# Kernel optimization log

Measured on AMD Instinct MI355X. Metric: run time of the kernel, lower is better.

The kernel has to match this reference:

```python
import jax, jax.numpy as jnp
import numpy as np

N_NODES = 50000
N_EDGES = 800000
IN_CH = 64
HID_CH = 64
OUT_CH = 64
NUM_GRAPHS = 256


def setup_inputs() -> dict:
    key = jax.random.key(0)
    ks = jax.random.split(key, 9)
    x = jax.random.normal(ks[0], (N_NODES, IN_CH), dtype=jnp.float32)
    edge_index = jax.random.randint(ks[1], (2, N_EDGES), 0, N_NODES, dtype=jnp.int64)
    batch = jnp.sort(jax.random.randint(ks[2], (N_NODES,), 0, NUM_GRAPHS, dtype=jnp.int64))
    def glorot(k, fan_in, fan_out):
        s = jnp.sqrt(6.0 / (fan_in + fan_out))
        return jax.random.uniform(k, (fan_in, fan_out), jnp.float32, -s, s)
    W1 = glorot(ks[3], IN_CH, HID_CH)
    b1 = jnp.zeros((HID_CH,), jnp.float32)
    W2 = glorot(ks[4], HID_CH, HID_CH)
    b2 = jnp.zeros((HID_CH,), jnp.float32)
    W3 = glorot(ks[5], HID_CH, OUT_CH)
    b3 = jnp.zeros((OUT_CH,), jnp.float32)
    return {"x": x, "edge_index": edge_index, "batch": batch,
            "W1": W1, "b1": b1, "W2": W2, "b2": b2, "W3": W3, "b3": b3}


def gcn_conv(x, src, dst, W, b):
    # PyG GCNConv: linear, add self-loops, symmetric deg normalization, scatter-add, bias
    n = x.shape[0]
    xw = x @ W                                   # [N, F_out]
    loops = jnp.arange(n, dtype=src.dtype)
    s = jnp.concatenate([src, loops])            # sources (with self loops)
    d = jnp.concatenate([dst, loops])            # targets (with self loops)
    ones = jnp.ones(d.shape, dtype=x.dtype)
    deg = jax.ops.segment_sum(ones, d, num_segments=n)
    dinv = jnp.where(deg > 0, jax.lax.rsqrt(deg), 0.0)
    norm = dinv[s] * dinv[d]                     # [E + N]
    msgs = norm[:, None] * xw[s]                 # gather + scale
    out = jax.ops.segment_sum(msgs, d, num_segments=n)
    return out + b


def reference(x, edge_index, batch, W1, b1, W2, b2, W3, b3):
    src, dst = edge_index[0], edge_index[1]
    h = jax.nn.relu(gcn_conv(x, src, dst, W1, b1))
    h = jax.nn.relu(gcn_conv(h, src, dst, W2, b2))
    h = gcn_conv(h, src, dst, W3, b3)
    # global_add_pool over graph ids
    pooled = jax.ops.segment_sum(h, batch, num_segments=NUM_GRAPHS)  # [G, OUT_CH]
    return pooled  # out_channels != 1, so no flatten
```

## Files before the change

### kernel.cpp

```cpp
#include <hip/hip_runtime.h>
#include <hip/hip_bf16.h>

#define N_NODES 50000
#define N_EDGES 800000
#define CH 64
#define N_GRAPHS 256
#define NBUCK 196
#define CHUNK 4096
#define NHIST 98

__device__ __forceinline__ unsigned bf16_rne(float f) {
    unsigned u = __float_as_uint(f);
    return (u + 0x7fffu + ((u >> 16) & 1u)) >> 16;
}
__device__ __forceinline__ float4 ldtab(const unsigned short* __restrict__ tab, int s, int c4) {
    uint2 u = *(const uint2*)(tab + ((size_t)s << 6) + c4);
    float4 r;
    r.x = __uint_as_float(u.x << 16);
    r.y = __uint_as_float(u.x & 0xffff0000u);
    r.z = __uint_as_float(u.y << 16);
    r.w = __uint_as_float(u.y & 0xffff0000u);
    return r;
}

__global__ void edge_hist(const int* __restrict__ ei, int* __restrict__ hpart) {
    __shared__ int h[NBUCK];
    for (int i = threadIdx.x; i < NBUCK; i += 256) h[i] = 0;
    __syncthreads();
    int t = blockIdx.x * 256 + threadIdx.x;
    int stride = NHIST * 256 * 4;
    for (int e = t * 4; e < N_EDGES; e += stride) {
        int4 d = *(const int4*)&ei[N_EDGES + e];
        atomicAdd(&h[d.x >> 8], 1);
        atomicAdd(&h[d.y >> 8], 1);
        atomicAdd(&h[d.z >> 8], 1);
        atomicAdd(&h[d.w >> 8], 1);
    }
    __syncthreads();
    for (int i = threadIdx.x; i < NBUCK; i += 256)
        hpart[blockIdx.x * NBUCK + i] = h[i];
}

__global__ void bucket_scan(const int* __restrict__ hpart, int* __restrict__ bstart,
                            int* __restrict__ gcur, float* __restrict__ poolz) {
    int i = blockIdx.x * 256 + threadIdx.x;
    if (i < N_GRAPHS * CH + N_GRAPHS) poolz[i] = 0.0f;
    if (blockIdx.x != 0) return;
    __shared__ int sc[256];
    int tid = threadIdx.x;
    int v = 0;
    if (tid < NBUCK)
        for (int r = 0; r < NHIST; ++r) v += hpart[r * NBUCK + tid];
    sc[tid] = v;
    __syncthreads();
    for (int off = 1; off < 256; off <<= 1) {
        int t = (tid >= off) ? sc[tid - off] : 0;
        __syncthreads();
        sc[tid] += t;
        __syncthreads();
    }
    if (tid < NBUCK) {
        int ex = sc[tid] - v;
        bstart[tid] = ex;
        gcur[tid] = ex;
    }
    if (tid == 255) bstart[NBUCK] = sc[255];
}

__global__ __launch_bounds__(512) void bin_scatter(const int* __restrict__ ei,
                                                   int* __restrict__ gcur,
                                                   int2* __restrict__ ebuf) {
    __shared__ int hist[NBUCK];
    __shared__ int lofs[NBUCK];
    __shared__ int gbase[NBUCK];
    __shared__ int cur[NBUCK];
    __shared__ int sc[512];
    __shared__ int2 stage[CHUNK];
    int tid = threadIdx.x;
    for (int i = tid; i < NBUCK; i += 512) hist[i] = 0;
    __syncthreads();
    int e0 = blockIdx.x * CHUNK;
    int n = min(CHUNK, N_EDGES - e0);
    int src[8], dst[8];
#pragma unroll
    for (int k = 0; k < 8; ++k) {
        int idx = k * 512 + tid;
        if (idx < n) {
            int e = e0 + idx;
            src[k] = ei[e];
            dst[k] = ei[N_EDGES + e];
            atomicAdd(&hist[dst[k] >> 8], 1);
        } else dst[k] = -1;
    }
    __syncthreads();
    int v = (tid < NBUCK) ? hist[tid] : 0;
    sc[tid] = v;
    __syncthreads();
    for (int off = 1; off < 512; off <<= 1) {
        int t = (tid >= off) ? sc[tid - off] : 0;
        __syncthreads();
        sc[tid] += t;
        __syncthreads();
    }
    if (tid < NBUCK) {
        int ex = sc[tid] - v;
        lofs[tid] = ex;
        cur[tid] = ex;
        gbase[tid] = v ? atomicAdd(&gcur[tid], v) : 0;
    }
    __syncthreads();
#pragma unroll
    for (int k = 0; k < 8; ++k) {
        if (dst[k] >= 0) {
            int p = atomicAdd(&cur[dst[k] >> 8], 1);
            stage[p] = make_int2(src[k], dst[k]);
        }
    }
    __syncthreads();
    for (int i = tid; i < n; i += 512) {
        int2 p = stage[i];
        int b = p.y >> 8;
        ebuf[gbase[b] + (i - lofs[b])] = p;
    }
}

__global__ void csr_bucket(const int2* __restrict__ ebuf, const int* __restrict__ bstart,
                           int* __restrict__ deg, int* __restrict__ rowp,
                           float* __restrict__ dinv, int* __restrict__ col) {
    __shared__ int nd[256];
    __shared__ int cur[256];
    __shared__ int sc[256];
    int b = blockIdx.x;
    int tid = threadIdx.x;
    nd[tid] = 0;
    __syncthreads();
    int es = bstart[b], ee = bstart[b + 1];
    for (int e = es + tid; e < ee; e += 256)
        atomicAdd(&nd[ebuf[e].y & 255], 1);
    __syncthreads();
    int v = nd[tid];
    sc[tid] = v;
    __syncthreads();
    for (int off = 1; off < 256; off <<= 1) {
        int t = (tid >= off) ? sc[tid - off] : 0;
        __syncthreads();
        sc[tid] += t;
        __syncthreads();
    }
    int node = b * 256 + tid;
    int lstart = es + sc[tid] - v;
    if (node < N_NODES) {
        deg[node] = v;
        rowp[node] = lstart;
        dinv[node] = rsqrtf((float)v + 1.0f);
    }
    cur[tid] = lstart;
    __syncthreads();
    for (int e = es + tid; e < ee; e += 256) {
        int2 p = ebuf[e];
        int pos = atomicAdd(&cur[p.y & 255], 1);
        col[pos] = p.x;
    }
}

__global__ void gemm_reg(const float* __restrict__ in, const float* __restrict__ W,
                         unsigned short* __restrict__ out, int n) {
    __shared__ float WT[64 * 68];
    int tid = threadIdx.x;
    for (int i = tid; i < 64 * 64; i += 256) {
        int k = i >> 6, c = i & 63;
        WT[c * 68 + k] = W[i];
    }
    __syncthreads();
    int lane = tid & 63;
    int wv = __builtin_amdgcn_readfirstlane(tid >> 6);
    int row0 = blockIdx.x * 32 + wv * 8;
    if (row0 >= n) return;
    float acc[8] = {0.f, 0.f, 0.f, 0.f, 0.f, 0.f, 0.f, 0.f};
#pragma unroll 2
    for (int k = 0; k < 64; k += 4) {
        float4 w = *(const float4*)&WT[lane * 68 + k];
#pragma unroll
        for (int r = 0; r < 8; ++r) {
            float4 xv = *(const float4*)&in[(size_t)(row0 + r) * 64 + k];
            acc[r] = fmaf(xv.x, w.x, acc[r]);
            acc[r] = fmaf(xv.y, w.y, acc[r]);
            acc[r] = fmaf(xv.z, w.z, acc[r]);
            acc[r] = fmaf(xv.w, w.w, acc[r]);
        }
    }
#pragma unroll
    for (int r = 0; r < 8; ++r)
        out[(size_t)(row0 + r) * 64 + lane] = (unsigned short)bf16_rne(acc[r]);
}

template <int OUT_BF16, int USE_NRM, int WRITE_NRM>
__global__ void agg_v4(const int* __restrict__ rowp, const int* __restrict__ deg,
                       const int* __restrict__ col, const float* __restrict__ dinv,
                       float* nrm,
                       const unsigned short* __restrict__ tab, const float* __restrict__ bias,
                       void* __restrict__ outv, int do_relu) {
    int wv = __builtin_amdgcn_readfirstlane(threadIdx.x >> 6);
    int node = blockIdx.x * 4 + wv;
    int lane = threadIdx.x & 63;
    int q = lane >> 4;
    int c4 = (lane & 15) << 2;
    float dd = dinv[node];
    int cnt = deg[node];
    int start = rowp[node];
    float4 acc = make_float4(0.f, 0.f, 0.f, 0.f);
    if (q == 0) {
        float4 xs = ldtab(tab, node, c4);
        float dd2 = dd * dd;
        acc.x = xs.x * dd2; acc.y = xs.y * dd2; acc.z = xs.z * dd2; acc.w = xs.w * dd2;
    }
    int j = 0;
    for (; j + 8 <= cnt; j += 8) {
        int sA = col[start + j + q];
        int sB = col[start + j + 4 + q];
        float nA, nB;
        if (USE_NRM) {
            nA = nrm[start + j + q];
            nB = nrm[start + j + 4 + q];
        } else {
            nA = dinv[sA] * dd;
            nB = dinv[sB] * dd;
        }
        float4 xA = ldtab(tab, sA, c4);
        float4 xB = ldtab(tab, sB, c4);
        if (WRITE_NRM && (lane & 15) == 0) {
            nrm[start + j + q] = nA;
            nrm[start + j + 4 + q] = nB;
        }
        acc.x = fmaf(nA, xA.x, acc.x); acc.y = fmaf(nA, xA.y, acc.y);
        acc.z = fmaf(nA, xA.z, acc.z); acc.w = fmaf(nA, xA.w, acc.w);
        acc.x = fmaf(nB, xB.x, acc.x); acc.y = fmaf(nB, xB.y, acc.y);
        acc.z = fmaf(nB, xB.z, acc.z); acc.w = fmaf(nB, xB.w, acc.w);
    }
    for (; j < cnt; j += 4) {
        int jj = j + q;
        bool valid = jj < cnt;
        int s = col[start + (valid ? jj : 0)];
        float nv;
        if (USE_NRM) {
            nv = valid ? nrm[start + jj] : 0.0f;
        } else {
            nv = valid ? dinv[s] * dd : 0.0f;
        }
        if (WRITE_NRM && valid && (lane & 15) == 0) nrm[start + jj] = nv;
        float4 xv = ldtab(tab, s, c4);
        acc.x = fmaf(nv, xv.x, acc.x); acc.y = fmaf(nv, xv.y, acc.y);
        acc.z = fmaf(nv, xv.z, acc.z); acc.w = fmaf(nv, xv.w, acc.w);
    }
    acc.x += __shfl_xor(acc.x, 16); acc.y += __shfl_xor(acc.y, 16);
    acc.z += __shfl_xor(acc.z, 16); acc.w += __shfl_xor(acc.w, 16);
    acc.x += __shfl_xor(acc.x, 32); acc.y += __shfl_xor(acc.y, 32);
    acc.z += __shfl_xor(acc.z, 32); acc.w += __shfl_xor(acc.w, 32);
    if (q == 0) {
        if (bias) {
            float4 bv = *(const float4*)&bias[c4];
            acc.x += bv.x; acc.y += bv.y; acc.z += bv.z; acc.w += bv.w;
        }
        if (do_relu) {
            acc.x = fmaxf(acc.x, 0.f); acc.y = fmaxf(acc.y, 0.f);
            acc.z = fmaxf(acc.z, 0.f); acc.w = fmaxf(acc.w, 0.f);
        }
        if (OUT_BF16) {
            uint2 o;
            o.x = bf16_rne(acc.x) | (bf16_rne(acc.y) << 16);
            o.y = bf16_rne(acc.z) | (bf16_rne(acc.w) << 16);
            *(uint2*)&((unsigned short*)outv)[((size_t)node << 6) + c4] = o;
        } else {
            *(float4*)&((float*)outv)[((size_t)node << 6) + c4] = acc;
        }
    }
}

__global__ void pool_seg(const float* __restrict__ h, const int* __restrict__ batch,
                         float* __restrict__ pool, float* __restrict__ cntg) {
    int ch = threadIdx.x & 63;
    int grp = threadIdx.x >> 6;
    int base = (blockIdx.x * 4 + grp) * 16;
    float acc = 0.0f;
    int curg = -1, runlen = 0;
    for (int n = 0; n < 16; ++n) {
        int node = base + n;
        if (node >= N_NODES) break;
        int g = batch[node];
        float v = h[((size_t)node << 6) + ch];
        if (g != curg) {
            if (curg >= 0) {
                atomicAdd(&pool[curg * 64 + ch], acc);
                if (ch == 0) atomicAdd(&cntg[curg], (float)runlen);
            }
            curg = g; acc = v; runlen = 1;
        } else { acc += v; runlen++; }
    }
    if (curg >= 0) {
        atomicAdd(&pool[curg * 64 + ch], acc);
        if (ch == 0) atomicAdd(&cntg[curg], (float)runlen);
    }
}

__global__ void out_gemm(const float* __restrict__ P, const float* __restrict__ cntg,
                         const float* __restrict__ W, const float* __restrict__ b,
                         float* __restrict__ out) {
    __shared__ float Ws[64 * 64];
    int tid = threadIdx.x;
    for (int i = tid; i < 64 * 64; i += 256) Ws[i] = W[i];
    __syncthreads();
    int lane = tid & 63;
    int g = blockIdx.x * 4 + (tid >> 6);
    if (g >= N_GRAPHS) return;
    float pv = P[g * 64 + lane];
    float acc = 0.0f;
#pragma unroll
    for (int k = 0; k < 64; ++k)
        acc = fmaf(__shfl(pv, k, 64), Ws[k * 64 + lane], acc);
    out[g * 64 + lane] = acc + cntg[g] * b[lane];
}

extern "C" void kernel_launch(void* const* d_in, const int* in_sizes, int n_in,
                              void* d_out, int out_size, void* d_ws, size_t ws_size,
                              hipStream_t stream) {
    const float* x   = (const float*)d_in[0];
    const int* ei    = (const int*)d_in[1];
    const int* batch = (const int*)d_in[2];
    const float* W1  = (const float*)d_in[3];
    const float* b1  = (const float*)d_in[4];
    const float* W2  = (const float*)d_in[5];
    const float* b2  = (const float*)d_in[6];
    const float* W3  = (const float*)d_in[7];
    const float* b3  = (const float*)d_in[8];
    float* out = (float*)d_out;

    char* ws = (char*)d_ws;
    float* dinv  = (float*)(ws);
    int*   DEG   = (int*)(ws + 200192);
    int*   ROWP  = (int*)(ws + 400384);
    int*   COL   = (int*)(ws + 600576);
    float* NRM   = (float*)(ws + 3800576);
    int*   HPART = (int*)(ws + 7000576);
    int*   BST   = (int*)(ws + 7077888);
    int*   GCUR  = (int*)(ws + 7078912);
    float* XW    = (float*)(ws + 7080960);
    int2*  EBUF  = (int2*)(ws + 7080960);
    float* ACC   = (float*)(ws + 19880960);
    float* POOL  = (float*)(ws + 32680960);
    float* CNT   = (float*)(ws + 32746496);

    const int WAVE_NODE_BLK = N_NODES / 4;
    const int GEMM_BLK = (N_NODES + 31) / 32;
    const int SCAT_BLK = (N_EDGES + CHUNK - 1) / CHUNK;

    edge_hist<<<NHIST, 256, 0, stream>>>(ei, HPART);
    bucket_scan<<<65, 256, 0, stream>>>(HPART, BST, GCUR, POOL);
    bin_scatter<<<SCAT_BLK, 512, 0, stream>>>(ei, GCUR, EBUF);
    csr_bucket<<<NBUCK, 256, 0, stream>>>(EBUF, BST, DEG, ROWP, dinv, COL);

    gemm_reg<<<GEMM_BLK, 256, 0, stream>>>(x, W1, (unsigned short*)XW, N_NODES);
    agg_v4<0, 0, 1><<<WAVE_NODE_BLK, 256, 0, stream>>>(ROWP, DEG, COL, dinv, NRM,
        (const unsigned short*)XW, b1, ACC, 1);

    gemm_reg<<<GEMM_BLK, 256, 0, stream>>>(ACC, W2, (unsigned short*)XW, N_NODES);
    agg_v4<1, 1, 0><<<WAVE_NODE_BLK, 256, 0, stream>>>(ROWP, DEG, COL, dinv, NRM,
        (const unsigned short*)XW, b2, ACC, 1);

    agg_v4<0, 1, 0><<<WAVE_NODE_BLK, 256, 0, stream>>>(ROWP, DEG, COL, dinv, NRM,
        (const unsigned short*)ACC, nullptr, XW, 0);
    pool_seg<<<(N_NODES + 63) / 64, 256, 0, stream>>>(XW, batch, POOL, CNT);
    out_gemm<<<N_GRAPHS / 4, 256, 0, stream>>>(POOL, CNT, W3, b3, out);
}
```

Before: 241.6 us.

## Pack edge source and fp16 norm into 32-bit words, bf16 final output

Edge records in binning are compressed from int2 to a single 32-bit word holding source, local destination and bucket. The first aggregation writes a packed array of 16-bit source index plus fp16 normalization, which later layers read instead of separate col and nrm arrays. The last aggregation emits bf16, which pooling reads. This cuts memory traffic on the bandwidth-bound gather passes, at the cost of reduced precision in norms and final features, and it relies on the node count fitting in 16 bits.

Measured after the change: 242.2 us. No clear change (+0.3%).

```diff
diff --git a/kernel.cpp b/kernel.cpp
--- a/kernel.cpp
+++ b/kernel.cpp
@@ -1,5 +1,6 @@
 #include <hip/hip_runtime.h>
 #include <hip/hip_bf16.h>
+#include <hip/hip_fp16.h>
 
 #define N_NODES 50000
 #define N_EDGES 800000
@@ -22,6 +23,12 @@
     r.w = __uint_as_float(u.y & 0xffff0000u);
     return r;
 }
+__device__ __forceinline__ unsigned pack_sn(int s, float n) {
+    return (unsigned)s | ((unsigned)__half_as_ushort(__float2half_rn(n)) << 16);
+}
+__device__ __forceinline__ float unpack_n(unsigned p) {
+    return __half2float(__ushort_as_half((unsigned short)(p >> 16)));
+}
 
 __global__ void edge_hist(const int* __restrict__ ei, int* __restrict__ hpart) {
     __shared__ int h[NBUCK];
@@ -69,13 +76,13 @@
 
 __global__ __launch_bounds__(512) void bin_scatter(const int* __restrict__ ei,
                                                    int* __restrict__ gcur,
-                                                   int2* __restrict__ ebuf) {
+                                                   unsigned* __restrict__ ebuf) {
     __shared__ int hist[NBUCK];
     __shared__ int lofs[NBUCK];
     __shared__ int gbase[NBUCK];
     __shared__ int cur[NBUCK];
     __shared__ int sc[512];
-    __shared__ int2 stage[CHUNK];
+    __shared__ unsigned stage[CHUNK];
     int tid = threadIdx.x;
     for (int i = tid; i < NBUCK; i += 512) hist[i] = 0;
     __syncthreads();
@@ -112,19 +119,21 @@
 #pragma unroll
     for (int k = 0; k < 8; ++k) {
         if (dst[k] >= 0) {
-            int p = atomicAdd(&cur[dst[k] >> 8], 1);
-            stage[p] = make_int2(src[k], dst[k]);
+            int b = dst[k] >> 8;
+            int p = atomicAdd(&cur[b], 1);
+            stage[p] = (unsigned)src[k] | ((unsigned)(dst[k] & 255) << 16)
+                                        | ((unsigned)b << 24);
         }
     }
     __syncthreads();
     for (int i = tid; i < n; i += 512) {
-        int2 p = stage[i];
-        int b = p.y >> 8;
+        unsigned p = stage[i];
+        int b = p >> 24;
         ebuf[gbase[b] + (i - lofs[b])] = p;
     }
 }
 
-__global__ void csr_bucket(const int2* __restrict__ ebuf, const int* __restrict__ bstart,
+__global__ void csr_bucket(const unsigned* __restrict__ ebuf, const int* __restrict__ bstart,
                            int* __restrict__ deg, int* __restrict__ rowp,
                            float* __restrict__ dinv, int* __restrict__ col) {
     __shared__ int nd[256];
@@ -136,7 +145,7 @@
     __syncthreads();
     int es = bstart[b], ee = bstart[b + 1];
     for (int e = es + tid; e < ee; e += 256)
-        atomicAdd(&nd[ebuf[e].y & 255], 1);
+        atomicAdd(&nd[(ebuf[e] >> 16) & 255], 1);
     __syncthreads();
     int v = nd[tid];
     sc[tid] = v;
@@ -157,9 +166,9 @@
     cur[tid] = lstart;
     __syncthreads();
     for (int e = es + tid; e < ee; e += 256) {
-        int2 p = ebuf[e];
-        int pos = atomicAdd(&cur[p.y & 255], 1);
-        col[pos] = p.x;
+        unsigned p = ebuf[e];
+        int pos = atomicAdd(&cur[(p >> 16) & 255], 1);
+        col[pos] = (int)(p & 0xFFFFu);
     }
 }
 
@@ -194,10 +203,10 @@
         out[(size_t)(row0 + r) * 64 + lane] = (unsigned short)bf16_rne(acc[r]);
 }
 
-template <int OUT_BF16, int USE_NRM, int WRITE_NRM>
+template <int OUT_BF16, int USE_PCK, int WRITE_PCK>
 __global__ void agg_v4(const int* __restrict__ rowp, const int* __restrict__ deg,
                        const int* __restrict__ col, const float* __restrict__ dinv,
-                       float* nrm,
+                       unsigned* __restrict__ pck,
                        const unsigned short* __restrict__ tab, const float* __restrict__ bias,
                        void* __restrict__ outv, int do_relu) {
     int wv = __builtin_amdgcn_readfirstlane(threadIdx.x >> 6);
@@ -216,21 +225,24 @@
     }
     int j = 0;
     for (; j + 8 <= cnt; j += 8) {
-        int sA = col[start + j + q];
-        int sB = col[start + j + 4 + q];
+        int sA, sB;
         float nA, nB;
-        if (USE_NRM) {
-            nA = nrm[start + j + q];
-            nB = nrm[start + j + 4 + q];
+        if (USE_PCK) {
+            unsigned pA = pck[start + j + q];
+            unsigned pB = pck[start + j + 4 + q];
+            sA = (int)(pA & 0xFFFFu); nA = unpack_n(pA);
+            sB = (int)(pB & 0xFFFFu); nB = unpack_n(pB);
         } else {
+            sA = col[start + j + q];
+            sB = col[start + j + 4 + q];
             nA = dinv[sA] * dd;
             nB = dinv[sB] * dd;
         }
         float4 xA = ldtab(tab, sA, c4);
         float4 xB = ldtab(tab, sB, c4);
-        if (WRITE_NRM && (lane & 15) == 0) {
-            nrm[start + j + q] = nA;
-            nrm[start + j + 4 + q] = nB;
+        if (WRITE_PCK && (lane & 15) == 0) {
+            pck[start + j + q] = pack_sn(sA, nA);
+            pck[start + j + 4 + q] = pack_sn(sB, nB);
         }
         acc.x = fmaf(nA, xA.x, acc.x); acc.y = fmaf(nA, xA.y, acc.y);
         acc.z = fmaf(nA, xA.z, acc.z); acc.w = fmaf(nA, xA.w, acc.w);
@@ -240,14 +252,18 @@
     for (; j < cnt; j += 4) {
         int jj = j + q;
         bool valid = jj < cnt;
-        int s = col[start + (valid ? jj : 0)];
+        int s;
         float nv;
-        if (USE_NRM) {
-            nv = valid ? nrm[start + jj] : 0.0f;
+        if (USE_PCK) {
+            unsigned p = pck[start + (valid ? jj : 0)];
+            s = (int)(p & 0xFFFFu);
+            nv = valid ? unpack_n(p) : 0.0f;
         } else {
+            s = col[start + (valid ? jj : 0)];
             nv = valid ? dinv[s] * dd : 0.0f;
-        }
-        if (WRITE_NRM && valid && (lane & 15) == 0) nrm[start + jj] = nv;
+            if (WRITE_PCK && valid && (lane & 15) == 0)
+                pck[start + jj] = pack_sn(s, nv);
+        }
         float4 xv = ldtab(tab, s, c4);
         acc.x = fmaf(nv, xv.x, acc.x); acc.y = fmaf(nv, xv.y, acc.y);
         acc.z = fmaf(nv, xv.z, acc.z); acc.w = fmaf(nv, xv.w, acc.w);
@@ -276,7 +292,7 @@
     }
 }
 
-__global__ void pool_seg(const float* __restrict__ h, const int* __restrict__ batch,
+__global__ void pool_seg(const unsigned short* __restrict__ h, const int* __restrict__ batch,
                          float* __restrict__ pool, float* __restrict__ cntg) {
     int ch = threadIdx.x & 63;
     int grp = threadIdx.x >> 6;
@@ -287,7 +303,7 @@
         int node = base + n;
         if (node >= N_NODES) break;
         int g = batch[node];
-        float v = h[((size_t)node << 6) + ch];
+        float v = __uint_as_float(((unsigned)h[((size_t)node << 6) + ch]) << 16);
         if (g != curg) {
             if (curg >= 0) {
                 atomicAdd(&pool[curg * 64 + ch], acc);
@@ -335,19 +351,19 @@
     float* out = (float*)d_out;
 
     char* ws = (char*)d_ws;
-    float* dinv  = (float*)(ws);
-    int*   DEG   = (int*)(ws + 200192);
-    int*   ROWP  = (int*)(ws + 400384);
-    int*   COL   = (int*)(ws + 600576);
-    float* NRM   = (float*)(ws + 3800576);
-    int*   HPART = (int*)(ws + 7000576);
-    int*   BST   = (int*)(ws + 7077888);
-    int*   GCUR  = (int*)(ws + 7078912);
-    float* XW    = (float*)(ws + 7080960);
-    int2*  EBUF  = (int2*)(ws + 7080960);
-    float* ACC   = (float*)(ws + 19880960);
-    float* POOL  = (float*)(ws + 32680960);
-    float* CNT   = (float*)(ws + 32746496);
+    float*    dinv  = (float*)(ws);
+    int*      DEG   = (int*)(ws + 200192);
+    int*      ROWP  = (int*)(ws + 400384);
+    int*      COL   = (int*)(ws + 600576);
+    unsigned* PCK   = (unsigned*)(ws + 3800576);
+    int*      HPART = (int*)(ws + 7000576);
+    int*      BST   = (int*)(ws + 7077888);
+    int*      GCUR  = (int*)(ws + 7078912);
+    float*    XW    = (float*)(ws + 7080960);
+    unsigned* EBUF  = (unsigned*)(ws + 7080960);
+    float*    ACC   = (float*)(ws + 19880960);
+    float*    POOL  = (float*)(ws + 32680960);
+    float*    CNT   = (float*)(ws + 32746496);
 
     const int WAVE_NODE_BLK = N_NODES / 4;
     const int GEMM_BLK = (N_NODES + 31) / 32;
@@ -359,15 +375,16 @@
     csr_bucket<<<NBUCK, 256, 0, stream>>>(EBUF, BST, DEG, ROWP, dinv, COL);
 
     gemm_reg<<<GEMM_BLK, 256, 0, stream>>>(x, W1, (unsigned short*)XW, N_NODES);
-    agg_v4<0, 0, 1><<<WAVE_NODE_BLK, 256, 0, stream>>>(ROWP, DEG, COL, dinv, NRM,
+    agg_v4<0, 0, 1><<<WAVE_NODE_BLK, 256, 0, stream>>>(ROWP, DEG, COL, dinv, PCK,
         (const unsigned short*)XW, b1, ACC, 1);
 
     gemm_reg<<<GEMM_BLK, 256, 0, stream>>>(ACC, W2, (unsigned short*)XW, N_NODES);
-    agg_v4<1, 1, 0><<<WAVE_NODE_BLK, 256, 0, stream>>>(ROWP, DEG, COL, dinv, NRM,
+    agg_v4<1, 1, 0><<<WAVE_NODE_BLK, 256, 0, stream>>>(ROWP, DEG, COL, dinv, PCK,
         (const unsigned short*)XW, b2, ACC, 1);
 
-    agg_v4<0, 1, 0><<<WAVE_NODE_BLK, 256, 0, stream>>>(ROWP, DEG, COL, dinv, NRM,
+    agg_v4<1, 1, 0><<<WAVE_NODE_BLK, 256, 0, stream>>>(ROWP, DEG, COL, dinv, PCK,
         (const unsigned short*)ACC, nullptr, XW, 0);
-    pool_seg<<<(N_NODES + 63) / 64, 256, 0, stream>>>(XW, batch, POOL, CNT);
+    pool_seg<<<(N_NODES + 63) / 64, 256, 0, stream>>>((const unsigned short*)XW,
+        batch, POOL, CNT);
     out_gemm<<<N_GRAPHS / 4, 256, 0, stream>>>(POOL, CNT, W3, b3, out);
 }
```
